# Optimization experiments

Measured on AMD Instinct MI355X. Metric: run time of the kernel, lower is better.

## Reference

```python
import jax, jax.numpy as jnp
import numpy as np

B, H, T, D = 4, 8, 8192, 64
NUM_CLUSTERS = 64
WINDOW_SIZE = 128
COMMITMENT = 1e-4
TOKEN_SELF_ATTN_VALUE = -50000.0
EPS = 1e-5


def l2norm(x, axis=-1):
    return x / jnp.linalg.norm(x, axis=axis, keepdims=True).clip(1e-12)


def shift(x):
    # relative->absolute position shift; x: (..., i, j) with i == j == wsz
    *lead, i, j = x.shape
    zero_pad = jnp.zeros((*lead, i, i), dtype=x.dtype)
    x = jnp.concatenate([x, zero_pad], axis=-1)          # (..., i, j+i)
    l = i + j - 1
    x = x.reshape(*lead, i * (i + j))
    pad = (-x.shape[-1]) % l
    if pad:
        x = jnp.concatenate([x, jnp.zeros((*lead, pad), dtype=x.dtype)], axis=-1)
    x = x.reshape(*lead, -1, l)
    return x[..., :i, i - 1:]


def setup_inputs() -> dict:
    key = jax.random.key(0)
    k1, k2, k3, k4 = jax.random.split(key, 4)
    qk = jax.random.normal(k1, (B, H, T, D), dtype=jnp.float32)
    v = jax.random.normal(k2, (B, H, T, D), dtype=jnp.float32)
    means = jax.random.normal(k3, (H, NUM_CLUSTERS, D), dtype=jnp.float32)
    rel_weights = jax.random.normal(k4, (WINDOW_SIZE, H, D), dtype=jnp.float32)
    return {"qk": qk, "v": v, "means": means, "rel_weights": rel_weights}


def reference(qk, v, means, rel_weights):
    b, h, t, d = qk.shape
    wsz = min(WINDOW_SIZE, t)
    nc = NUM_CLUSTERS
    scale = d ** -0.5

    # --- kmeans routing (eval: no iterations, fixed means) ---
    k_routing = l2norm(qk)                                        # bhtd
    means_ng = jax.lax.stop_gradient(means)
    dists = jnp.einsum('bhld,hcd->bhlc', jax.lax.stop_gradient(k_routing), means_ng)
    buckets = jnp.argmax(dists, axis=-1)                          # bht
    # top-wsz tokens per cluster, sorted by position
    _, topk_idx = jax.lax.top_k(dists.transpose(0, 1, 3, 2), wsz)  # bhc,wsz
    indices = jnp.sort(topk_idx, axis=-1).reshape(b, h, nc * wsz)  # bhN

    # commitment loss (grad flows only through k_routing, means is a buffer)
    routed_means = means_ng[jnp.arange(h)[None, :, None], buckets]  # bhtd
    commitment_loss = jnp.mean((k_routing - routed_means) ** 2) * COMMITMENT

    # --- gather tokens per cluster ---
    qk_g = jnp.take_along_axis(qk, indices[..., None], axis=2).reshape(b, h, nc, wsz, d)
    v_g = jnp.take_along_axis(v, indices[..., None], axis=2).reshape(b, h, nc, wsz, d)

    q = qk_g
    k = l2norm(qk_g)
    dots = jnp.einsum('bhnid,bhnjd->bhnij', q, k) * scale

    # relative positional bias
    rel = jnp.einsum('bhnid,jhd->bhnij', q, rel_weights) * scale
    dots = dots + shift(rel)

    # mask self-attention on the diagonal
    eye = jnp.eye(wsz, dtype=bool)
    dots = jnp.where(eye, TOKEN_SELF_ATTN_VALUE, dots)

    attn = jax.nn.softmax(dots, axis=-1)
    bo = jnp.einsum('bhnij,bhnjd->bhnid', attn, v_g)
    so = bo.reshape(b, h, nc * wsz, d)

    # --- scatter-mean back to sequence positions ---
    N = nc * wsz
    flat_idx = (jnp.arange(b * h)[:, None] * t + indices.reshape(b * h, N)).reshape(-1)
    so_flat = so.reshape(b * h * N, d)
    numer = jax.ops.segment_sum(so_flat, flat_idx, num_segments=b * h * t)
    denom = jax.ops.segment_sum(jnp.ones((b * h * N,), so.dtype), flat_idx, num_segments=b * h * t)
    out = (numer / (denom[:, None] + EPS)).reshape(b, h, t, d)

    return out, commitment_loss
```

## Files before the change

### kernel.cpp

```cpp
#include <hip/hip_runtime.h>
#include <math.h>

typedef _Float16 h16;
typedef _Float16 f16x8 __attribute__((ext_vector_type(8)));
typedef float f32x4 __attribute__((ext_vector_type(4)));

#define Bc 4
#define Hc 8
#define Tc 8192
#define Dc 64
#define NCc 64
#define WSZc 128
#define BHc (Bc*Hc)
#define MAXPc 16
#define OVFCAP 4095
#define OUT_ELEMS (16777216u)

#define MFMA16(a,b,c) __builtin_amdgcn_mfma_f32_16x16x32_f16(a,b,c,0,0,0)

__global__ __launch_bounds__(256) void k_dists(const float* __restrict__ qk,
                                               const float* __restrict__ means,
                                               float* __restrict__ dists,
                                               float* __restrict__ loss_acc) {
    __shared__ float sm[NCc*Dc];
    __shared__ float red[4];
    int tid = threadIdx.x;
    int blk = blockIdx.x;
    int bh  = blk >> 5;
    int chunk = blk & 31;
    int h = bh & (Hc-1);

    const float* mh = means + (size_t)h*NCc*Dc;
    for (int i = tid; i < NCc*Dc; i += 256) sm[i] = mh[i];
    __syncthreads();

    int t = chunk*256 + tid;
    const float* qrow = qk + ((size_t)bh*Tc + t)*Dc;
    float q[Dc];
    #pragma unroll
    for (int d = 0; d < Dc; d += 4) {
        float4 f = *(const float4*)(qrow + d);
        q[d] = f.x; q[d+1] = f.y; q[d+2] = f.z; q[d+3] = f.w;
    }
    float n2 = 0.f;
    #pragma unroll
    for (int d = 0; d < Dc; d++) n2 += q[d]*q[d];
    float nrm = sqrtf(n2);
    if (nrm < 1e-12f) nrm = 1e-12f;
    float inv = 1.0f/nrm;

    float best = -3.4e38f; int bc = 0;
    float* dbase = dists + ((size_t)bh*NCc)*Tc + (size_t)chunk*256 + tid;
    for (int c = 0; c < NCc; c++) {
        float acc = 0.f;
        const float* mc = sm + c*Dc;
        #pragma unroll
        for (int d = 0; d < Dc; d++) acc += q[d]*mc[d];
        float dv = acc*inv;
        dbase[(size_t)c*Tc] = dv;
        if (dv > best) { best = dv; bc = c; }
    }
    float ls = 0.f;
    const float* mb = sm + bc*Dc;
    #pragma unroll
    for (int d = 0; d < Dc; d++) {
        float diff = q[d]*inv - mb[d];
        ls += diff*diff;
    }
    float lf = ls;
    #pragma unroll
    for (int o = 32; o >= 1; o >>= 1) lf += __shfl_down(lf, o, 64);
    if ((tid & 63) == 0) red[tid >> 6] = lf;
    __syncthreads();
    if (tid == 0) atomicAdd(loss_acc, red[0]+red[1]+red[2]+red[3]);
}

__device__ inline unsigned blockScanIncl(unsigned v, volatile unsigned* wsum,
                                         int lane, int wid, unsigned* ptotal) {
    unsigned x = v;
    #pragma unroll
    for (int s = 1; s < 64; s <<= 1) {
        unsigned o = __shfl_up(x, s, 64);
        if (lane >= s) x += o;
    }
    if (lane == 63) wsum[wid] = x;
    __syncthreads();
    unsigned off = 0, tot = 0;
    #pragma unroll
    for (int w2 = 0; w2 < 4; w2++) {
        unsigned s2 = wsum[w2];
        if (w2 < wid) off += s2;
        tot += s2;
    }
    *ptotal = tot;
    return x + off;
}

__global__ __launch_bounds__(256, 6) void k_topk(const float* __restrict__ dists,
                                              int* __restrict__ indices,
                                              unsigned* __restrict__ cnt,
                                              unsigned short* __restrict__ slots,
                                              unsigned* __restrict__ aux) {
    __shared__ unsigned hist[4096];
    __shared__ unsigned bmap[256];
    __shared__ unsigned eqbuf[256];
    __shared__ unsigned wsum[4];
    __shared__ unsigned sh_prefix;
    __shared__ int      sh_k, cnt_eq;

    int tid = threadIdx.x;
    int lane = tid & 63, wid = tid >> 6;
    int bhc = blockIdx.x, bh = bhc >> 6, c = bhc & 63;
    const float* dp = dists + (size_t)bhc*Tc;

    for (int i = tid; i < 4096; i += 256) hist[i] = 0u;
    if (tid == 0) { sh_k = WSZc; sh_prefix = 0u; cnt_eq = 0; }
    bmap[tid] = 0u;
    __syncthreads();

    unsigned key[8][4];
    #pragma unroll
    for (int ch = 0; ch < 8; ch++) {
        float4 f = *(const float4*)(dp + ch*1024 + tid*4);
        float fv[4] = {f.x, f.y, f.z, f.w};
        #pragma unroll
        for (int j = 0; j < 4; j++) {
            unsigned u = __float_as_uint(fv[j]);
            u = (u & 0x80000000u) ? ~u : (u | 0x80000000u);
            key[ch][j] = u;
            atomicAdd(&hist[u >> 20], 1u);
        }
    }
    __syncthreads();

    unsigned prefix = 0u; int k = WSZc;
    #pragma unroll
    for (int lvl = 0; lvl < 3; lvl++) {
        const int shift   = (lvl == 0) ? 20 : (lvl == 1 ? 8 : 0);
        const int nper    = (lvl == 2) ? 1 : 16;
        const unsigned nbm = (lvl == 2) ? 255u : 4095u;
        if (lvl > 0) {
            const unsigned maskH = (lvl == 1) ? 0xFFF00000u : 0xFFFFFF00u;
            for (int i = tid; i <= (int)nbm; i += 256) hist[i] = 0u;
            __syncthreads();
            #pragma unroll
            for (int ch = 0; ch < 8; ch++)
                #pragma unroll
                for (int j = 0; j < 4; j++) {
                    unsigned ky = key[ch][j];
                    if ((ky & maskH) == prefix)
                        atomicAdd(&hist[(ky >> shift) & nbm], 1u);
                }
            __syncthreads();
        }
        int tBase = tid*nper;
        unsigned psum = 0;
        for (int i = 0; i < nper; i++) psum += hist[tBase + i];
        unsigned total;
        unsigned incl = blockScanIncl(psum, wsum, lane, wid, &total);
        unsigned beyond = total - incl;
        unsigned suff   = beyond + psum;
        if (beyond < (unsigned)k && (unsigned)k <= suff) {
            unsigned run = beyond;
            for (int i = nper - 1; i >= 0; i--) {
                unsigned hb = hist[tBase + i];
                run += hb;
                if (run >= (unsigned)k) {
                    sh_prefix = prefix | ((unsigned)(tBase + i) << shift);
                    sh_k = k - (int)(run - hb);
                    break;
                }
            }
        }
        __syncthreads();
        prefix = sh_prefix; k = sh_k;
        __syncthreads();
    }
    unsigned Kthr = prefix;
    int kEq = k;

    #pragma unroll
    for (int ch = 0; ch < 8; ch++)
        #pragma unroll
        for (int j = 0; j < 4; j++) {
            unsigned ky = key[ch][j];
            int t = ch*1024 + tid*4 + j;
            if (ky > Kthr) atomicOr(&bmap[t >> 5], 1u << (t & 31));
            else if (ky == Kthr) {
                int p = atomicAdd(&cnt_eq, 1);
                if (p < 256) eqbuf[p] = (unsigned)t;
            }
        }
    __syncthreads();
    if (cnt_eq == kEq) {
        if (tid < kEq) {
            unsigned t = eqbuf[tid];
            atomicOr(&bmap[t >> 5], 1u << (t & 31));
        }
    } else {
        int ce = cnt_eq < 256 ? cnt_eq : 256;
        if (tid >= ce) eqbuf[tid] = 0xFFFFFFFFu;
        __syncthreads();
        for (int k2 = 2; k2 <= 256; k2 <<= 1) {
            for (int j = k2 >> 1; j >= 1; j >>= 1) {
                int i = tid, ixj = i ^ j;
                if (ixj > i) {
                    bool up = ((i & k2) == 0);
                    unsigned a = eqbuf[i], b = eqbuf[ixj];
                    if ((a > b) == up) { eqbuf[i] = b; eqbuf[ixj] = a; }
                }
                __syncthreads();
            }
        }
        if (tid < kEq) {
            unsigned t = eqbuf[tid];
            atomicOr(&bmap[t >> 5], 1u << (t & 31));
        }
    }
    __syncthreads();

    unsigned w = bmap[tid];
    int pc = __popc(w);
    unsigned total2;
    unsigned incl2 = blockScanIncl((unsigned)pc, wsum, lane, wid, &total2);
    int pos = (int)(incl2 - pc);
    while (w) {
        int b = __ffs(w) - 1; w &= w - 1;
        int t = tid*32 + b;
        indices[(size_t)bhc*WSZc + pos] = t;
        unsigned row = ((unsigned)bh << 13) + (unsigned)t;
        unsigned p2 = atomicAdd(&cnt[row], 1u);
        if (p2 < MAXPc) slots[(size_t)row*MAXPc + p2] = (unsigned short)(c*128 + pos);
        else {
            unsigned o = atomicAdd(&aux[0], 1u);
            if (o < OVFCAP) aux[2+o] = (unsigned)(bhc*WSZc + pos);
        }
        pos++;
    }
}

__global__ __launch_bounds__(256, 3) void k_attn(const float* __restrict__ qk,
                                                 const float* __restrict__ v,
                                                 const float* __restrict__ relw,
                                                 const int* __restrict__ indices,
                                                 float* __restrict__ bo) {
    __shared__ __align__(16) h16 qv[128*72];
    __shared__ __align__(16) h16 sp[128*136];
    __shared__ float sinv[128];

    int tid = threadIdx.x;
    int bid = blockIdx.x;
    int bhc = ((bid & 7) << 8) | (bid >> 3);
    int bh = bhc >> 6, h = bh & (Hc-1);
    int lane = tid & 63, wid = tid >> 6;
    int quad = lane >> 4, lj = lane & 15;
    int i0 = wid*32;

    int myIdx = indices[(size_t)bhc*WSZc + (tid >> 1)];

    {
        int i = tid >> 1, hf = tid & 1;
        const float* qrow = qk + ((size_t)bh*Tc + myIdx)*Dc + hf*32;
        float n2 = 0.f;
        #pragma unroll
        for (int k8 = 0; k8 < 4; k8++) {
            float4 a = *(const float4*)(qrow + k8*8);
            float4 b = *(const float4*)(qrow + k8*8 + 4);
            n2 += a.x*a.x + a.y*a.y + a.z*a.z + a.w*a.w
                + b.x*b.x + b.y*b.y + b.z*b.z + b.w*b.w;
            f16x8 hq = {(h16)a.x,(h16)a.y,(h16)a.z,(h16)a.w,
                        (h16)b.x,(h16)b.y,(h16)b.z,(h16)b.w};
            *(f16x8*)&qv[i*72 + hf*32 + k8*8] = hq;
        }
        n2 += __shfl_xor(n2, 1, 64);
        if (hf == 0) {
            float nr = sqrtf(n2); if (nr < 1e-12f) nr = 1e-12f;
            sinv[i] = 0.125f / nr;
        }
    }
    __syncthreads();

    {
        const float* wh = relw + (size_t)h*Dc;
        #pragma unroll
        for (int mt = 0; mt < 2; mt++) {
            int ntMin = (mt == 0 ? 7 : 6) - 2*wid;
            f32x4 accR[8];
            #pragma unroll
            for (int nt = 0; nt < 8; nt++)
                #pragma unroll
                for (int e = 0; e < 4; e++) accR[nt][e] = 0.f;
            #pragma unroll
            for (int k0 = 0; k0 < 64; k0 += 32) {
                f16x8 a = *(const f16x8*)&qv[(i0 + mt*16 + lj)*72 + k0 + quad*8];
                #pragma unroll
                for (int nt = 0; nt < 8; nt++) {
                    if (nt < ntMin) continue;
                    const float* wp = wh + (size_t)(nt*16 + lj)*(Hc*Dc) + k0 + quad*8;
                    float4 wa = *(const float4*)wp;
                    float4 wc = *(const float4*)(wp + 4);
                    f16x8 bf = {(h16)wa.x,(h16)wa.y,(h16)wa.z,(h16)wa.w,
                                (h16)wc.x,(h16)wc.y,(h16)wc.z,(h16)wc.w};
                    accR[nt] = MFMA16(a, bf, accR[nt]);
                }
            }
            #pragma unroll
            for (int nt = 0; nt < 8; nt++) {
                if (nt < ntMin) continue;
                #pragma unroll
                for (int r = 0; r < 4; r++) {
                    int i = i0 + mt*16 + quad*4 + r;
                    int j = nt*16 + lj - 127 + i;
                    if (j >= 0) sp[i*136 + j] = (h16)(accR[nt][r] * 0.125f);
                }
            }
        }
    }

    f16x8 vh[4];
    {
        int hf = tid & 1;
        const float* vrow = v + ((size_t)bh*Tc + myIdx)*Dc + hf*32;
        #pragma unroll
        for (int r = 0; r < 4; r++) {
            float4 a = *(const float4*)(vrow + r*8);
            float4 b = *(const float4*)(vrow + r*8 + 4);
            f16x8 hv = {(h16)a.x,(h16)a.y,(h16)a.z,(h16)a.w,
                        (h16)b.x,(h16)b.y,(h16)b.z,(h16)b.w};
            vh[r] = hv;
        }
    }

    f32x4 accS[2][8];
    #pragma unroll
    for (int mt = 0; mt < 2; mt++)
        #pragma unroll
        for (int nt = 0; nt < 8; nt++)
            #pragma unroll
            for (int e = 0; e < 4; e++) accS[mt][nt][e] = 0.f;
    #pragma unroll
    for (int k0 = 0; k0 < 64; k0 += 32) {
        f16x8 a0 = *(const f16x8*)&qv[(i0 + lj)*72 + k0 + quad*8];
        f16x8 a1 = *(const f16x8*)&qv[(i0 + 16 + lj)*72 + k0 + quad*8];
        #pragma unroll
        for (int nt = 0; nt < 8; nt++) {
            f16x8 bf = *(const f16x8*)&qv[(nt*16 + lj)*72 + k0 + quad*8];
            accS[0][nt] = MFMA16(a0, bf, accS[0][nt]);
            accS[1][nt] = MFMA16(a1, bf, accS[1][nt]);
        }
    }
    __syncthreads();

    #pragma unroll
    for (int nt = 0; nt < 8; nt++) {
        int j = nt*16 + lj;
        float sj = sinv[j];
        #pragma unroll
        for (int mt = 0; mt < 2; mt++)
            #pragma unroll
            for (int r = 0; r < 4; r++) {
                int i = i0 + mt*16 + quad*4 + r;
                float rl = (j <= i) ? (float)sp[i*136 + j] : 0.f;
                float s = accS[mt][nt][r]*sj + rl;
                accS[mt][nt][r] = (i == j) ? -50000.0f : s;
            }
    }
    #pragma unroll
    for (int mt = 0; mt < 2; mt++)
        #pragma unroll
        for (int r = 0; r < 4; r++) {
            float mx = accS[mt][0][r];
            #pragma unroll
            for (int nt = 1; nt < 8; nt++) mx = fmaxf(mx, accS[mt][nt][r]);
            #pragma unroll
            for (int st = 1; st <= 8; st <<= 1) mx = fmaxf(mx, __shfl_xor(mx, st, 64));
            float sum = 0.f;
            #pragma unroll
            for (int nt = 0; nt < 8; nt++) {
                float e = __expf(accS[mt][nt][r] - mx);
                accS[mt][nt][r] = e; sum += e;
            }
            #pragma unroll
            for (int st = 1; st <= 8; st <<= 1) sum += __shfl_xor(sum, st, 64);
            float inv = 1.0f/sum;
            #pragma unroll
            for (int nt = 0; nt < 8; nt++) accS[mt][nt][r] *= inv;
        }
    #pragma unroll
    for (int mt = 0; mt < 2; mt++)
        #pragma unroll
        for (int nt = 0; nt < 8; nt++)
            #pragma unroll
            for (int r = 0; r < 4; r++) {
                int i = i0 + mt*16 + quad*4 + r;
                sp[i*136 + nt*16 + lj] = (h16)accS[mt][nt][r];
            }
    {
        h16* vt = qv;
        int j = tid >> 1, hf = tid & 1;
        #pragma unroll
        for (int r = 0; r < 4; r++) {
            int d0 = hf*32 + r*8;
            #pragma unroll
            for (int e = 0; e < 8; e++)
                vt[(d0+e)*136 + j] = vh[r][e];
        }
    }
    __syncthreads();

    f32x4 accO[2][4];
    #pragma unroll
    for (int mt = 0; mt < 2; mt++)
        #pragma unroll
        for (int nt = 0; nt < 4; nt++)
            #pragma unroll
            for (int e = 0; e < 4; e++) accO[mt][nt][e] = 0.f;
    #pragma unroll
    for (int k0 = 0; k0 < 128; k0 += 32) {
        f16x8 a0 = *(const f16x8*)&sp[(i0 + lj)*136 + k0 + quad*8];
        f16x8 a1 = *(const f16x8*)&sp[(i0 + 16 + lj)*136 + k0 + quad*8];
        #pragma unroll
        for (int nt = 0; nt < 4; nt++) {
            f16x8 bf = *(const f16x8*)&qv[(nt*16 + lj)*136 + k0 + quad*8];
            accO[0][nt] = MFMA16(a0, bf, accO[0][nt]);
            accO[1][nt] = MFMA16(a1, bf, accO[1][nt]);
        }
    }
    #pragma unroll
    for (int mt = 0; mt < 2; mt++)
        #pragma unroll
        for (int nt = 0; nt < 4; nt++)
            #pragma unroll
            for (int r = 0; r < 4; r++) {
                int i = i0 + mt*16 + quad*4 + r;
                bo[((size_t)bhc*WSZc + i)*Dc + nt*16 + lj] = accO[mt][nt][r];
            }
}

__global__ __launch_bounds__(256) void k_final(const float* __restrict__ bo,
                                               const unsigned short* __restrict__ slots,
                                               const unsigned* __restrict__ cnt,
                                               const int* __restrict__ indices,
                                               const unsigned* __restrict__ aux,
                                               float* __restrict__ out) {
    int row  = blockIdx.x*4 + (threadIdx.x >> 6);
    int lane = threadIdx.x & 63;
    unsigned c = cnt[row];
    unsigned m = c < MAXPc ? c : MAXPc;
    int bh = row >> 13;
    float acc = 0.f;
    const unsigned short* sl = slots + (size_t)row*MAXPc;
    for (unsigned p = 0; p < m; p++)
        acc += bo[(((size_t)bh << 13) + sl[p])*Dc + lane];
    if (c > MAXPc) {
        unsigned n = aux[0]; if (n > OVFCAP) n = OVFCAP;
        int tok = row & 8191;
        for (unsigned q = 0; q < n; q++) {
            unsigned e = aux[2+q];
            if ((int)(e >> 13) == bh && indices[e] == tok)
                acc += bo[(((size_t)bh << 13) + (e & 8191))*Dc + lane];
        }
    }
    out[(size_t)row*Dc + lane] = acc * (1.0f/((float)c + 1e-5f));
    if (row == 0 && lane == 0)
        out[OUT_ELEMS] = ((const float*)aux)[1] * (float)(1e-4 / 16777216.0);
}

extern "C" void kernel_launch(void* const* d_in, const int* in_sizes, int n_in,
                              void* d_out, int out_size, void* d_ws, size_t ws_size,
                              hipStream_t stream) {
    const float* qk    = (const float*)d_in[0];
    const float* v     = (const float*)d_in[1];
    const float* means = (const float*)d_in[2];
    const float* relw  = (const float*)d_in[3];
    float* out = (float*)d_out;
    char*  ws  = (char*)d_ws;

    size_t off = 0;
    float* dists = (float*)(ws + off);
    float* bo    = dists;
    off += (size_t)BHc*NCc*Tc*4;
    int* indices = (int*)(ws + off); off += (size_t)BHc*NCc*WSZc*4;
    unsigned* cnt = (unsigned*)(ws + off); off += (size_t)BHc*Tc*4;
    unsigned* aux = (unsigned*)(ws + off); off += (size_t)(2+OVFCAP)*4;
    unsigned short* slots = (unsigned short*)(ws + off);
    off += (size_t)BHc*Tc*MAXPc*2;

    hipMemsetAsync(cnt, 0, (size_t)BHc*Tc*4 + (size_t)(2+OVFCAP)*4, stream);

    k_dists <<<BHc*(Tc/256), 256, 0, stream>>>(qk, means, dists, (float*)aux + 1);
    k_topk  <<<BHc*NCc,      256, 0, stream>>>(dists, indices, cnt, slots, aux);
    k_attn  <<<BHc*NCc,      256, 0, stream>>>(qk, v, relw, indices, bo);
    k_final <<<BHc*Tc/4,     256, 0, stream>>>(bo, slots, cnt, indices, aux, out);
}
```

Before: 394.2 us.

## Pre-pack relative weights to fp16 and share B-fragments across both M-tiles

Adds a small kernel that converts the relative-position weights to fp16 in a per-head contiguous layout once per call. The attention kernel then loads ready fp16 fragments instead of strided fp32 loads plus conversion, and each fragment feeds both 16-row M tiles, halving weight loads. This also drops the finer per-tile skip bound, so a few extra MFMAs run for the first tile. Launch bounds drop from 3 to 2 blocks per SM to fit the doubled accumulator set, which may reduce occupancy.

```diff
diff --git a/kernel.cpp b/kernel.cpp
--- a/kernel.cpp
+++ b/kernel.cpp
@@ -17,6 +17,19 @@
 #define OUT_ELEMS (16777216u)
 
 #define MFMA16(a,b,c) __builtin_amdgcn_mfma_f32_16x16x32_f16(a,b,c,0,0,0)
+
+__global__ __launch_bounds__(256) void k_wpack(const float* __restrict__ relw,
+                                               h16* __restrict__ wh16) {
+    int idx = blockIdx.x*256 + threadIdx.x;
+    int e = idx*8;
+    int m = e >> 9, h = (e >> 6) & 7, d = e & 63;
+    const float* src = relw + ((size_t)m*Hc + h)*Dc + d;
+    float4 a = *(const float4*)src;
+    float4 b = *(const float4*)(src + 4);
+    f16x8 hv = {(h16)a.x,(h16)a.y,(h16)a.z,(h16)a.w,
+                (h16)b.x,(h16)b.y,(h16)b.z,(h16)b.w};
+    *(f16x8*)&wh16[((size_t)h*WSZc + m)*Dc + d] = hv;
+}
 
 __global__ __launch_bounds__(256) void k_dists(const float* __restrict__ qk,
                                                const float* __restrict__ means,
@@ -239,9 +252,9 @@
     }
 }
 
-__global__ __launch_bounds__(256, 3) void k_attn(const float* __restrict__ qk,
+__global__ __launch_bounds__(256, 2) void k_attn(const float* __restrict__ qk,
                                                  const float* __restrict__ v,
-                                                 const float* __restrict__ relw,
+                                                 const h16* __restrict__ wh16,
                                                  const int* __restrict__ indices,
                                                  float* __restrict__ bo) {
     __shared__ __align__(16) h16 qv[128*72];
@@ -280,30 +293,30 @@
     }
     __syncthreads();
 
+    int ntMin = 6 - 2*wid;
     {
-        const float* wh = relw + (size_t)h*Dc;
-        #pragma unroll
-        for (int mt = 0; mt < 2; mt++) {
-            int ntMin = (mt == 0 ? 7 : 6) - 2*wid;
-            f32x4 accR[8];
+        f32x4 accR[2][8];
+        #pragma unroll
+        for (int mt = 0; mt < 2; mt++)
             #pragma unroll
             for (int nt = 0; nt < 8; nt++)
                 #pragma unroll
-                for (int e = 0; e < 4; e++) accR[nt][e] = 0.f;
-            #pragma unroll
-            for (int k0 = 0; k0 < 64; k0 += 32) {
-                f16x8 a = *(const f16x8*)&qv[(i0 + mt*16 + lj)*72 + k0 + quad*8];
-                #pragma unroll
-                for (int nt = 0; nt < 8; nt++) {
-                    if (nt < ntMin) continue;
-                    const float* wp = wh + (size_t)(nt*16 + lj)*(Hc*Dc) + k0 + quad*8;
-                    float4 wa = *(const float4*)wp;
-                    float4 wc = *(const float4*)(wp + 4);
-                    f16x8 bf = {(h16)wa.x,(h16)wa.y,(h16)wa.z,(h16)wa.w,
-                                (h16)wc.x,(h16)wc.y,(h16)wc.z,(h16)wc.w};
-                    accR[nt] = MFMA16(a, bf, accR[nt]);
-                }
-            }
+                for (int e = 0; e < 4; e++) accR[mt][nt][e] = 0.f;
+        const h16* whp = wh16 + (size_t)h*WSZc*Dc;
+        #pragma unroll
+        for (int k0 = 0; k0 < 64; k0 += 32) {
+            f16x8 a0 = *(const f16x8*)&qv[(i0 + lj)*72 + k0 + quad*8];
+            f16x8 a1 = *(const f16x8*)&qv[(i0 + 16 + lj)*72 + k0 + quad*8];
+            #pragma unroll
+            for (int nt = 0; nt < 8; nt++) {
+                if (nt < ntMin) continue;
+                f16x8 bf = *(const f16x8*)&whp[(size_t)(nt*16 + lj)*Dc + k0 + quad*8];
+                accR[0][nt] = MFMA16(a0, bf, accR[0][nt]);
+                accR[1][nt] = MFMA16(a1, bf, accR[1][nt]);
+            }
+        }
+        #pragma unroll
+        for (int mt = 0; mt < 2; mt++)
             #pragma unroll
             for (int nt = 0; nt < 8; nt++) {
                 if (nt < ntMin) continue;
@@ -311,10 +324,9 @@
                 for (int r = 0; r < 4; r++) {
                     int i = i0 + mt*16 + quad*4 + r;
                     int j = nt*16 + lj - 127 + i;
-                    if (j >= 0) sp[i*136 + j] = (h16)(accR[nt][r] * 0.125f);
+                    if (j >= 0) sp[i*136 + j] = (h16)(accR[mt][nt][r] * 0.125f);
                 }
             }
-        }
     }
 
     f16x8 vh[4];
@@ -485,11 +497,13 @@
     unsigned* aux = (unsigned*)(ws + off); off += (size_t)(2+OVFCAP)*4;
     unsigned short* slots = (unsigned short*)(ws + off);
     off += (size_t)BHc*Tc*MAXPc*2;
+    h16* wh16 = (h16*)(ws + off); off += (size_t)WSZc*Hc*Dc*2;
 
     hipMemsetAsync(cnt, 0, (size_t)BHc*Tc*4 + (size_t)(2+OVFCAP)*4, stream);
 
+    k_wpack <<<32,           256, 0, stream>>>(relw, wh16);
     k_dists <<<BHc*(Tc/256), 256, 0, stream>>>(qk, means, dists, (float*)aux + 1);
     k_topk  <<<BHc*NCc,      256, 0, stream>>>(dists, indices, cnt, slots, aux);
-    k_attn  <<<BHc*NCc,      256, 0, stream>>>(qk, v, relw, indices, bo);
+    k_attn  <<<BHc*NCc,      256, 0, stream>>>(qk, v, wh16, indices, bo);
     k_final <<<BHc*Tc/4,     256, 0, stream>>>(bo, slots, cnt, indices, aux, out);
 }
```

New measurement: 366.7 us. -7.0%, faster.
